# Optimization experiments

Measured on AMD Instinct MI355X. Metric: run time of the kernel, lower is better.

The kernel has to match this reference:

```python
import jax, jax.numpy as jnp
import numpy as np

B, N_CAM, J = 8, 5, 15        # batch, cameras, joints
H, W = 128, 240               # heatmap h, w  (HEATMAP_SIZE = [240, 128] = [w, h])
VX, VY, VZ = 80, 80, 20       # voxels_per_axis
NBINS = VX * VY * VZ          # 128000


def setup_inputs() -> dict:
    key = jax.random.key(0)
    k1, k2 = jax.random.split(key)
    heatmaps = jax.random.uniform(k1, (B, N_CAM, J, H, W), dtype=jnp.float32)
    # cached projected sampling grid, clamped to [-1.1, 1.1] as in project_grid
    sample_grid = jax.random.uniform(k2, (N_CAM, NBINS, 2), dtype=jnp.float32,
                                     minval=-1.1, maxval=1.1)
    return {"heatmaps": heatmaps, "sample_grid": sample_grid}


def _grid_sample_bilinear(hm, grid):
    """F.grid_sample(mode='bilinear', padding_mode='zeros', align_corners=True).

    hm:   [B, n, J, H, W]
    grid: [n, nbins, 2]  normalized (x, y) in roughly [-1.1, 1.1]
    returns [B, n, J, nbins]
    """
    Bv, n, Jv, Hv, Wv = hm.shape
    nb = grid.shape[1]
    gx, gy = grid[..., 0], grid[..., 1]
    # align_corners=True mapping from [-1, 1] to pixel coords
    ix = (gx + 1.0) * 0.5 * (Wv - 1)
    iy = (gy + 1.0) * 0.5 * (Hv - 1)
    x0 = jnp.floor(ix)
    y0 = jnp.floor(iy)
    x1 = x0 + 1.0
    y1 = y0 + 1.0
    wx1 = ix - x0
    wx0 = 1.0 - wx1
    wy1 = iy - y0
    wy0 = 1.0 - wy1

    hmf = hm.reshape(Bv, n, Jv, Hv * Wv)

    def gather(yi, xi):
        # zeros padding: out-of-range corners contribute 0
        valid = ((xi >= 0) & (xi <= Wv - 1) & (yi >= 0) & (yi <= Hv - 1))
        xc = jnp.clip(xi, 0, Wv - 1).astype(jnp.int32)
        yc = jnp.clip(yi, 0, Hv - 1).astype(jnp.int32)
        idx = yc * Wv + xc                                   # [n, nb]
        idxb = jnp.broadcast_to(idx[None, :, None, :], (Bv, n, Jv, nb))
        vals = jnp.take_along_axis(hmf, idxb, axis=3)        # [B, n, J, nb]
        return vals * valid[None, :, None, :].astype(hm.dtype)

    out = (gather(y0, x0) * (wy0 * wx0)[None, :, None, :]
           + gather(y0, x1) * (wy0 * wx1)[None, :, None, :]
           + gather(y1, x0) * (wy1 * wx0)[None, :, None, :]
           + gather(y1, x1) * (wy1 * wx1)[None, :, None, :])
    return out


def reference(heatmaps, sample_grid):
    sampled = _grid_sample_bilinear(heatmaps, sample_grid)   # [B, n, J, nbins]
    cubes = jnp.clip(jnp.mean(sampled, axis=1), 0.0, 1.0)    # mean over cameras
    return cubes.reshape(heatmaps.shape[0], heatmaps.shape[2], VX, VY, VZ)
```

## Files before the change

### kernel.cpp

```cpp
#include <hip/hip_runtime.h>
#include <hip/hip_fp16.h>

#define B_     8
#define NCAM   5
#define J_     15
#define H_     128
#define W_     240
#define NB     128000
#define HW_    (H_ * W_)
#define PAIR_ROWS (H_ / 2)
#define PAIR_DW  (PAIR_ROWS * W_)
#define SMEM_BYTES (PAIR_DW * 4)
#define PAIR_G4  (PAIR_DW / 4)
#define TPB    1024
#define NCHUNK 8
#define BPB    (NB / NCHUNK)
#define ITEMS  16
#define NBJ    (B_ * J_)
#define NBLK   (NBJ * NCHUNK)

typedef __fp16 fp16x2 __attribute__((ext_vector_type(2)));

__device__ __forceinline__ unsigned int pkrtz(float lo, float hi) {
    fp16x2 h = __builtin_amdgcn_cvt_pkrtz(lo, hi);
    return __builtin_bit_cast(unsigned int, h);
}

__device__ __forceinline__ void bilinear_rec(float gx, float gy,
                                             unsigned int& addr,
                                             unsigned int& w0pk,
                                             unsigned int& w1pk) {
    const float ix = (gx + 1.0f) * (0.5f * (W_ - 1));
    const float iy = (gy + 1.0f) * (0.5f * (H_ - 1));
    const float x0f = floorf(ix);
    const float y0f = floorf(iy);
    const float wx1 = ix - x0f, wx0 = 1.0f - wx1;
    const float wy1 = iy - y0f, wy0 = 1.0f - wy1;
    const int x0 = (int)x0f;
    const int y0 = (int)y0f;
    const int xc = min(max(x0, 0), W_ - 2);
    const int yc = min(max(y0, 0), H_ - 2);
    const float vx0 = (x0 >= 0  && x0 <= W_ - 1) ? wx0 : 0.0f;
    const float vx1 = (x0 >= -1 && x0 <= W_ - 2) ? wx1 : 0.0f;
    const float vy0 = (y0 >= 0  && y0 <= H_ - 1) ? wy0 : 0.0f;
    const float vy1 = (y0 >= -1 && y0 <= H_ - 2) ? wy1 : 0.0f;
    const bool xhi = (x0 == W_ - 1);
    const bool xlo = (x0 == -1);
    const bool yhi = (y0 == H_ - 1);
    const bool ylo = (y0 == -1);
    const float a0 = (xhi ? 0.0f : vx0) + (xlo ? vx1 : 0.0f);
    const float a1 = (xhi ? vx0 : 0.0f) + (xlo ? 0.0f : vx1);
    const float b0 = (yhi ? 0.0f : vy0) + (ylo ? vy1 : 0.0f);
    const float b1 = (yhi ? vy0 : 0.0f) + (ylo ? 0.0f : vy1);
    const int yp  = yc >> 1;
    const int odd = yc & 1;
    addr = (unsigned int)(yp * W_ + xc) | ((unsigned int)odd << 14);
    w0pk = pkrtz(0.2f * (a0 * b0), 0.2f * (a0 * b1));
    w1pk = pkrtz(0.2f * (a1 * b0), 0.2f * (a1 * b1));
}

__global__ __launch_bounds__(256) void weights_kernel(
    const float* __restrict__ sgrid,
    unsigned short* __restrict__ addr16,
    uint2* __restrict__ wpk)
{
    const int i = blockIdx.x * 256 + threadIdx.x;
    if (i >= NCAM * NB) return;
    const float2 g = ((const float2*)sgrid)[i];
    unsigned int a, w0, w1;
    bilinear_rec(g.x, g.y, a, w0, w1);
    addr16[i] = (unsigned short)a;
    wpk[i] = make_uint2(w0, w1);
}

__device__ __forceinline__ void stage_pairs(const float* __restrict__ img,
                                            unsigned int* s_img, int tid) {
    const float4* __restrict__ src4 = (const float4*)img;
    uint4* dst = (uint4*)s_img;
    for (int gi = tid; gi < PAIR_G4; gi += TPB) {
        const int y2 = gi / (W_ / 4);
        const int xg = gi - y2 * (W_ / 4);
        const float4 t  = src4[120 * y2 + xg];
        const float4 bo = src4[120 * y2 + 60 + xg];
        uint4 d;
        d.x = pkrtz(t.x, bo.x);
        d.y = pkrtz(t.y, bo.y);
        d.z = pkrtz(t.z, bo.z);
        d.w = pkrtz(t.w, bo.w);
        dst[gi] = d;
    }
}

__device__ __forceinline__ float sample_pair(const unsigned int* s_img,
                                             unsigned int a16,
                                             unsigned int w0, unsigned int w1) {
    const unsigned int odd = a16 >> 14;
    const unsigned int a   = a16 & 0x3FFFu;
    const unsigned int sel = 0x03020100u + odd * 0x02020202u;
    const unsigned int* base = s_img + a;
    const unsigned int d_a0 = base[0];
    const unsigned int d_a1 = base[1];
    const unsigned int off  = odd * (unsigned int)W_;
    const unsigned int d_b0 = base[off];
    const unsigned int d_b1 = base[off + 1];
    const unsigned int c0 = __builtin_amdgcn_perm(d_b0, d_a0, sel);
    const unsigned int c1 = __builtin_amdgcn_perm(d_b1, d_a1, sel);
    __half2 p = __hmul2(__builtin_bit_cast(__half2, c0),
                        __builtin_bit_cast(__half2, w0));
    p = __hfma2(__builtin_bit_cast(__half2, c1),
                __builtin_bit_cast(__half2, w1), p);
    return __low2float(p) + __high2float(p);
}

__global__ __launch_bounds__(TPB, 8) void project_kernel(
    const float* __restrict__ hm,
    const unsigned short* __restrict__ addr16,
    const uint2* __restrict__ wpk,
    float* __restrict__ out)
{
    extern __shared__ unsigned int s_img[];
    const int tid   = threadIdx.x;
    const int bj    = blockIdx.x % NBJ;
    const int chunk = blockIdx.x / NBJ;
    const int b     = bj / J_;
    const int j     = bj % J_;
    const int bin0  = chunk * BPB;

    float acc[ITEMS];
#pragma unroll
    for (int it = 0; it < ITEMS; ++it) acc[it] = 0.0f;

    for (int n = 0; n < NCAM; ++n) {
        __syncthreads();
        stage_pairs(hm + (((size_t)b * NCAM + n) * J_ + j) * HW_, s_img, tid);
        __syncthreads();
        const unsigned short* __restrict__ ap = addr16 + n * NB + bin0;
        const uint2* __restrict__ wp = wpk + n * NB + bin0;
#pragma unroll
        for (int it = 0; it < ITEMS; ++it) {
            const int r = it * TPB + tid;
            if (r < BPB) {
                acc[it] += sample_pair(s_img, ap[r], wp[r].x, wp[r].y);
            }
        }
    }

    float* __restrict__ o = out + (size_t)bj * NB + bin0;
#pragma unroll
    for (int it = 0; it < ITEMS; ++it) {
        const int r = it * TPB + tid;
        if (r < BPB) o[r] = fminf(fmaxf(acc[it], 0.0f), 1.0f);
    }
}

#define FB_SMEM   (HW_ * 4)
#define FB_NCHUNK 5
#define FB_BPB    (NB / FB_NCHUNK)
#define FB_ITEMS  (FB_BPB / TPB)
__global__ __launch_bounds__(TPB) void project_fallback(
    const float* __restrict__ hm,
    const float* __restrict__ sgrid,
    float* __restrict__ out)
{
    extern __shared__ float s_f32[];
    const int tid   = threadIdx.x;
    const int bj    = blockIdx.x % NBJ;
    const int chunk = blockIdx.x / NBJ;
    const int b     = bj / J_;
    const int j     = bj % J_;
    const int bin0  = chunk * FB_BPB;

    float acc[FB_ITEMS];
#pragma unroll
    for (int it = 0; it < FB_ITEMS; ++it) acc[it] = 0.0f;

    for (int n = 0; n < NCAM; ++n) {
        __syncthreads();
        const float4* __restrict__ src =
            (const float4*)(hm + (((size_t)b * NCAM + n) * J_ + j) * HW_);
        float4* dst = (float4*)s_f32;
        for (int i = tid; i < HW_ / 4; i += TPB) dst[i] = src[i];
        __syncthreads();
        const float2* __restrict__ g2 = (const float2*)sgrid + n * NB + bin0;
#pragma unroll
        for (int it = 0; it < FB_ITEMS; ++it) {
            const float2 g = g2[it * TPB + tid];
            const float ix = (g.x + 1.0f) * (0.5f * (W_ - 1));
            const float iy = (g.y + 1.0f) * (0.5f * (H_ - 1));
            const float x0f = floorf(ix), y0f = floorf(iy);
            const float wx1 = ix - x0f, wx0 = 1.0f - wx1;
            const float wy1 = iy - y0f, wy0 = 1.0f - wy1;
            const int x0 = (int)x0f, y0 = (int)y0f;
            const int xc = min(max(x0, 0), W_ - 2);
            const int yc = min(max(y0, 0), H_ - 2);
            const float vx0 = (x0 >= 0  && x0 <= W_ - 1) ? wx0 : 0.0f;
            const float vx1 = (x0 >= -1 && x0 <= W_ - 2) ? wx1 : 0.0f;
            const float vy0 = (y0 >= 0  && y0 <= H_ - 1) ? wy0 : 0.0f;
            const float vy1 = (y0 >= -1 && y0 <= H_ - 2) ? wy1 : 0.0f;
            const bool xhi = (x0 == W_ - 1), xlo = (x0 == -1);
            const bool yhi = (y0 == H_ - 1), ylo = (y0 == -1);
            const float a0 = (xhi ? 0.0f : vx0) + (xlo ? vx1 : 0.0f);
            const float a1 = (xhi ? vx0 : 0.0f) + (xlo ? 0.0f : vx1);
            const float b0 = (yhi ? 0.0f : vy0) + (ylo ? vy1 : 0.0f);
            const float b1 = (yhi ? vy0 : 0.0f) + (ylo ? 0.0f : vy1);
            const float* r0 = s_f32 + (yc * W_ + xc);
            acc[it] += b0 * (a0 * r0[0] + a1 * r0[1])
                     + b1 * (a0 * r0[W_] + a1 * r0[W_ + 1]);
        }
    }
    float* __restrict__ o = out + (size_t)bj * NB + bin0;
#pragma unroll
    for (int it = 0; it < FB_ITEMS; ++it)
        o[it * TPB + tid] = fminf(fmaxf(acc[it] * 0.2f, 0.0f), 1.0f);
}

extern "C" void kernel_launch(void* const* d_in, const int* in_sizes, int n_in,
                              void* d_out, int out_size, void* d_ws, size_t ws_size,
                              hipStream_t stream) {
    const float* hm = (const float*)d_in[0];
    const float* sg = (const float*)d_in[1];
    float* out = (float*)d_out;

    (void)hipFuncSetAttribute((const void*)project_fallback,
                              hipFuncAttributeMaxDynamicSharedMemorySize, FB_SMEM);

    const size_t addr_bytes = (size_t)NCAM * NB * sizeof(unsigned short);
    const size_t wpk_bytes  = (size_t)NCAM * NB * sizeof(uint2);
    if (ws_size >= addr_bytes + wpk_bytes) {
        unsigned short* addr16 = (unsigned short*)d_ws;
        uint2* wpk = (uint2*)((char*)d_ws + addr_bytes);
        weights_kernel<<<(NCAM * NB + 255) / 256, 256, 0, stream>>>(sg, addr16, wpk);
        project_kernel<<<NBLK, TPB, SMEM_BYTES, stream>>>(hm, addr16, wpk, out);
    } else {
        project_fallback<<<NBJ * FB_NCHUNK, TPB, FB_SMEM, stream>>>(hm, sg, out);
    }
}
```

Before: 224.6 us.

## Stage horizontal fp16 pixel pairs in LDS instead of vertical row pairs

The shared-memory image layout changes from vertically paired rows to horizontally paired neighbours: each dword holds fp16 pixels (x, x+1) for every row. Each bilinear sample then needs only two LDS reads, with no byte permutes and no odd/even row decoding. Weights are repacked per row to match. The cost is that the staged image doubles to about 120 KB of LDS per block and staging writes twice as much. That likely limits residency to one 1024-thread block per CU and reduces overlap between staging and sampling.

```diff
diff --git a/kernel.cpp b/kernel.cpp
--- a/kernel.cpp
+++ b/kernel.cpp
@@ -8,10 +8,9 @@
 #define W_     240
 #define NB     128000
 #define HW_    (H_ * W_)
-#define PAIR_ROWS (H_ / 2)
-#define PAIR_DW  (PAIR_ROWS * W_)
-#define SMEM_BYTES (PAIR_DW * 4)
-#define PAIR_G4  (PAIR_DW / 4)
+#define IMG_DW   HW_
+#define SMEM_BYTES (IMG_DW * 4)
+#define IMG_G4   (IMG_DW / 4)
 #define TPB    1024
 #define NCHUNK 8
 #define BPB    (NB / NCHUNK)
@@ -28,8 +27,8 @@
 
 __device__ __forceinline__ void bilinear_rec(float gx, float gy,
                                              unsigned int& addr,
-                                             unsigned int& w0pk,
-                                             unsigned int& w1pk) {
+                                             unsigned int& wtop,
+                                             unsigned int& wbot) {
     const float ix = (gx + 1.0f) * (0.5f * (W_ - 1));
     const float iy = (gy + 1.0f) * (0.5f * (H_ - 1));
     const float x0f = floorf(ix);
@@ -52,11 +51,9 @@
     const float a1 = (xhi ? vx0 : 0.0f) + (xlo ? 0.0f : vx1);
     const float b0 = (yhi ? 0.0f : vy0) + (ylo ? vy1 : 0.0f);
     const float b1 = (yhi ? vy0 : 0.0f) + (ylo ? 0.0f : vy1);
-    const int yp  = yc >> 1;
-    const int odd = yc & 1;
-    addr = (unsigned int)(yp * W_ + xc) | ((unsigned int)odd << 14);
-    w0pk = pkrtz(0.2f * (a0 * b0), 0.2f * (a0 * b1));
-    w1pk = pkrtz(0.2f * (a1 * b0), 0.2f * (a1 * b1));
+    addr = (unsigned int)(yc * W_ + xc);
+    wtop = pkrtz(0.2f * (b0 * a0), 0.2f * (b0 * a1));
+    wbot = pkrtz(0.2f * (b1 * a0), 0.2f * (b1 * a1));
 }
 
 __global__ __launch_bounds__(256) void weights_kernel(
@@ -67,52 +64,42 @@
     const int i = blockIdx.x * 256 + threadIdx.x;
     if (i >= NCAM * NB) return;
     const float2 g = ((const float2*)sgrid)[i];
-    unsigned int a, w0, w1;
-    bilinear_rec(g.x, g.y, a, w0, w1);
+    unsigned int a, wt, wb;
+    bilinear_rec(g.x, g.y, a, wt, wb);
     addr16[i] = (unsigned short)a;
-    wpk[i] = make_uint2(w0, w1);
-}
-
-__device__ __forceinline__ void stage_pairs(const float* __restrict__ img,
-                                            unsigned int* s_img, int tid) {
+    wpk[i] = make_uint2(wt, wb);
+}
+
+__device__ __forceinline__ void stage_xpairs(const float* __restrict__ img,
+                                             unsigned int* s_img, int tid) {
     const float4* __restrict__ src4 = (const float4*)img;
     uint4* dst = (uint4*)s_img;
-    for (int gi = tid; gi < PAIR_G4; gi += TPB) {
-        const int y2 = gi / (W_ / 4);
-        const int xg = gi - y2 * (W_ / 4);
-        const float4 t  = src4[120 * y2 + xg];
-        const float4 bo = src4[120 * y2 + 60 + xg];
+    for (int g = tid; g < IMG_G4; g += TPB) {
+        const float4 a = src4[g];
+        const float  b = img[min(4 * g + 4, HW_ - 1)];
         uint4 d;
-        d.x = pkrtz(t.x, bo.x);
-        d.y = pkrtz(t.y, bo.y);
-        d.z = pkrtz(t.z, bo.z);
-        d.w = pkrtz(t.w, bo.w);
-        dst[gi] = d;
-    }
-}
-
-__device__ __forceinline__ float sample_pair(const unsigned int* s_img,
-                                             unsigned int a16,
-                                             unsigned int w0, unsigned int w1) {
-    const unsigned int odd = a16 >> 14;
-    const unsigned int a   = a16 & 0x3FFFu;
-    const unsigned int sel = 0x03020100u + odd * 0x02020202u;
+        d.x = pkrtz(a.x, a.y);
+        d.y = pkrtz(a.y, a.z);
+        d.z = pkrtz(a.z, a.w);
+        d.w = pkrtz(a.w, b);
+        dst[g] = d;
+    }
+}
+
+__device__ __forceinline__ float sample_xpair(const unsigned int* s_img,
+                                              unsigned int a,
+                                              unsigned int wtop, unsigned int wbot) {
     const unsigned int* base = s_img + a;
-    const unsigned int d_a0 = base[0];
-    const unsigned int d_a1 = base[1];
-    const unsigned int off  = odd * (unsigned int)W_;
-    const unsigned int d_b0 = base[off];
-    const unsigned int d_b1 = base[off + 1];
-    const unsigned int c0 = __builtin_amdgcn_perm(d_b0, d_a0, sel);
-    const unsigned int c1 = __builtin_amdgcn_perm(d_b1, d_a1, sel);
-    __half2 p = __hmul2(__builtin_bit_cast(__half2, c0),
-                        __builtin_bit_cast(__half2, w0));
-    p = __hfma2(__builtin_bit_cast(__half2, c1),
-                __builtin_bit_cast(__half2, w1), p);
+    const unsigned int d_top = base[0];
+    const unsigned int d_bot = base[W_];
+    __half2 p = __hmul2(__builtin_bit_cast(__half2, d_top),
+                        __builtin_bit_cast(__half2, wtop));
+    p = __hfma2(__builtin_bit_cast(__half2, d_bot),
+                __builtin_bit_cast(__half2, wbot), p);
     return __low2float(p) + __high2float(p);
 }
 
-__global__ __launch_bounds__(TPB, 8) void project_kernel(
+__global__ __launch_bounds__(TPB, 4) void project_kernel(
     const float* __restrict__ hm,
     const unsigned short* __restrict__ addr16,
     const uint2* __restrict__ wpk,
@@ -132,7 +119,7 @@
 
     for (int n = 0; n < NCAM; ++n) {
         __syncthreads();
-        stage_pairs(hm + (((size_t)b * NCAM + n) * J_ + j) * HW_, s_img, tid);
+        stage_xpairs(hm + (((size_t)b * NCAM + n) * J_ + j) * HW_, s_img, tid);
         __syncthreads();
         const unsigned short* __restrict__ ap = addr16 + n * NB + bin0;
         const uint2* __restrict__ wp = wpk + n * NB + bin0;
@@ -140,7 +127,7 @@
         for (int it = 0; it < ITEMS; ++it) {
             const int r = it * TPB + tid;
             if (r < BPB) {
-                acc[it] += sample_pair(s_img, ap[r], wp[r].x, wp[r].y);
+                acc[it] += sample_xpair(s_img, ap[r], wp[r].x, wp[r].y);
             }
         }
     }
@@ -221,6 +208,8 @@
     const float* sg = (const float*)d_in[1];
     float* out = (float*)d_out;
 
+    (void)hipFuncSetAttribute((const void*)project_kernel,
+                              hipFuncAttributeMaxDynamicSharedMemorySize, SMEM_BYTES);
     (void)hipFuncSetAttribute((const void*)project_fallback,
                               hipFuncAttributeMaxDynamicSharedMemorySize, FB_SMEM);
 
```

Result: slower. 233.2 us (+3.8%).
